# Kernel optimization log

Hardware: AMD Instinct MI355X
Metric: run time of the kernel (lower is better)

Reference implementation:

```python
import jax, jax.numpy as jnp
import numpy as np

NITER = 3

def fft2c(x):
    x = jnp.fft.ifftshift(x, axes=(-2, -1))
    x = jnp.fft.fft2(x, axes=(-2, -1), norm='ortho')
    return jnp.fft.fftshift(x, axes=(-2, -1))

def ifft2c(x):
    x = jnp.fft.ifftshift(x, axes=(-2, -1))
    x = jnp.fft.ifft2(x, axes=(-2, -1), norm='ortho')
    return jnp.fft.fftshift(x, axes=(-2, -1))

def conv3d(x, w):
    # x: [N, D, H, W, C]; w: [3,3,3,Cin,Cout]; 'same' padding, stride 1, no bias
    return jax.lax.conv_general_dilated(x, w, window_strides=(1, 1, 1), padding='SAME',
                                        dimension_numbers=('NDHWC', 'DHWIO', 'NDHWC'))

def setup_inputs():
    key = jax.random.key(0)
    ks = jax.random.split(key, 16)
    nb, nt, nx, ny = 1, 18, 160, 160
    s = 0.05  # weight scale to keep unrolled iterations numerically tame
    d_real = jax.random.normal(ks[0], (nb, nt, nx, ny), jnp.float32)
    d_imag = jax.random.normal(ks[1], (nb, nt, nx, ny), jnp.float32)
    mask = jax.random.randint(ks[2], (nt, nx, ny), 0, 2, jnp.int32)
    W1 = jax.random.normal(ks[3], (NITER, 3, 3, 3, 2, 16), jnp.float32) * s
    W2 = jax.random.normal(ks[4], (NITER, 3, 3, 3, 16, 16), jnp.float32) * s
    W3 = jax.random.normal(ks[5], (NITER, 3, 3, 3, 16, 16), jnp.float32) * s
    W4 = jax.random.normal(ks[6], (NITER, 3, 3, 3, 16, 16), jnp.float32) * s
    W5 = jax.random.normal(ks[7], (NITER, 3, 3, 3, 16, 16), jnp.float32) * s
    W6 = jax.random.normal(ks[8], (NITER, 3, 3, 3, 16, 2), jnp.float32) * s
    lam1 = jnp.full((NITER,), 0.1, jnp.float32)       # lambda_step init
    lam2 = jnp.full((NITER,), 0.1, jnp.float32)       # lambda_step_2 init
    soft_thr = jnp.full((NITER,), 0.1, jnp.float32)
    thres_coef = jnp.full((NITER,), -2.0, jnp.float32)
    eta = jnp.full((NITER,), 0.01, jnp.float32)
    return dict(d_real=d_real, d_imag=d_imag, mask=mask, W1=W1, W2=W2, W3=W3, W4=W4,
                W5=W5, W6=W6, lam1=lam1, lam2=lam2, soft_thr=soft_thr,
                thres_coef=thres_coef, eta=eta)

def _slr_net(d_real, d_imag, mask, W1, W2, W3, W4, W5, W6, lam1, lam2, soft_thr, thres_coef, eta):
    d = jax.lax.complex(d_real, d_imag)          # [nb,nt,nx,ny] complex64
    m = mask.astype(jnp.complex64)               # [nt,nx,ny], broadcasts over batch
    x_rec = ifft2c(d * m)                        # E^H d
    t = jnp.zeros_like(x_rec)
    beta = jnp.zeros_like(x_rec)
    X_SYM = []
    for i in range(NITER):
        lam = jnp.maximum(lam1[i], 0.0).astype(jnp.complex64)
        lam2c = jnp.maximum(lam2[i], 0.0).astype(jnp.complex64)
        # data-consistency gradient: E^H (E x - d)
        ATAX = ifft2c(m * (m * fft2c(x_rec) - d))
        r_n = x_rec - lam * ATAX + lam2c * (x_rec + beta - t)
        r = jnp.stack([r_n.real, r_n.imag], axis=-1)  # [nb,nt,nx,ny,2]
        x1 = jax.nn.relu(conv3d(r, W1[i]))
        x2 = jax.nn.relu(conv3d(x1, W2[i]))
        x3 = conv3d(x2, W3[i])
        x_soft = jnp.sign(x3) * jax.nn.relu(jnp.abs(x3) - soft_thr[i])
        x4 = jax.nn.relu(conv3d(x_soft, W4[i]))
        x5 = jax.nn.relu(conv3d(x4, W5[i]))
        x6 = conv3d(x5, W6[i])
        x_out = x6 + r
        xs = jax.nn.relu(conv3d(x3, W4[i]))
        xs = jax.nn.relu(conv3d(xs, W5[i]))
        xs = conv3d(xs, W6[i])
        x_sym = xs - r
        x_rec = jax.lax.complex(x_out[..., 0], x_out[..., 1])
        # low-rank step: batched thin SVD with learned singular-value thresholding
        nb_, nt_, nx_, ny_ = x_rec.shape
        M = x_rec.reshape(nb_, nt_, nx_ * ny_)
        U, S, Vh = jnp.linalg.svd(M, full_matrices=False)   # U:[b,nt,nt] S:[b,nt] Vh:[b,nt,nx*ny]
        thres = jax.nn.sigmoid(thres_coef[i]) * S[:, :1]
        S = jax.nn.relu(S - thres)
        t = (U * S[:, None, :].astype(U.dtype)) @ Vh
        t = t.reshape(nb_, nt_, nx_, ny_)
        beta = beta + jnp.maximum(eta[i], 0.0).astype(jnp.complex64) * (x_rec - t)
        X_SYM.append(x_sym)
    return x_rec, jnp.stack(X_SYM)

def reference(d_real, d_imag, mask, W1, W2, W3, W4, W5, W6, lam1, lam2, soft_thr, thres_coef, eta):
    return _slr_net(d_real, d_imag, mask, W1, W2, W3, W4, W5, W6, lam1, lam2, soft_thr, thres_coef, eta)
```

## Files before the change

kernel.cpp:

```cpp
#include <hip/hip_runtime.h>
#include <hip/hip_fp16.h>

#define NT 18
#define NX 160
#define NY 160
#define NPIX (NX*NY)
#define NVOX (NT*NPIX)

typedef _Float16 __attribute__((ext_vector_type(2))) half2t;
typedef _Float16 __attribute__((ext_vector_type(8))) half8t;
typedef float    __attribute__((ext_vector_type(4))) f32x4;
typedef unsigned int u32;
typedef __attribute__((address_space(1))) const u32 gu32;
typedef __attribute__((address_space(3))) u32 lu32;

__global__ void probe_kernel(float* __restrict__ out, int n, float val) {
  int i = blockIdx.x * 256 + threadIdx.x;
  if (i < n) out[i] = val;
}

__global__ void make_g_kernel(float2* __restrict__ G) {
  int idx = blockIdx.x * 256 + threadIdx.x;
  if (idx >= NPIX) return;
  int r = idx / NY, c = idx - (idx / NY) * NY;
  int rs = (r + 80) % 160;
  int cs = (c + 80) % 160;
  int prod = (rs * cs) % 160;
  double ang = -2.0 * 3.14159265358979323846 * (double)prod / 160.0;
  double sc = 0.07905694150420949;
  G[idx] = make_float2((float)(cos(ang) * sc), (float)(sin(ang) * sc));
}

__global__ void zero_kernel(float* __restrict__ p, int n) {
  int i = blockIdx.x * 256 + threadIdx.x;
  if (i < n) p[i] = 0.f;
}

template <int MASKD>
__global__ void fft_pass_last4(const float2* __restrict__ in, float2* __restrict__ out,
                               const float2* __restrict__ G, int conjf,
                               const float* __restrict__ dr, const float* __restrict__ di,
                               const int* __restrict__ maskp) {
  __shared__ float2 rows[4][NY];
  int r0 = blockIdx.x * 4;
  int v = threadIdx.x;
#pragma unroll
  for (int r = 0; r < 4; ++r) {
    size_t idx = (size_t)(r0 + r) * NY + v;
    if (MASKD) {
      float m = (float)maskp[idx];
      rows[r][v] = make_float2(m * dr[idx], m * di[idx]);
    } else {
      rows[r][v] = in[idx];
    }
  }
  __syncthreads();
  float sgn = conjf ? -1.f : 1.f;
  float ar[4] = {0.f, 0.f, 0.f, 0.f}, ai[4] = {0.f, 0.f, 0.f, 0.f};
  for (int k = 0; k < NY; ++k) {
    float2 g = G[k * NY + v];
    float gi = sgn * g.y;
#pragma unroll
    for (int r = 0; r < 4; ++r) {
      float2 a = rows[r][k];
      ar[r] += a.x * g.x - a.y * gi;
      ai[r] += a.x * gi + a.y * g.x;
    }
  }
#pragma unroll
  for (int r = 0; r < 4; ++r)
    out[(size_t)(r0 + r) * NY + v] = make_float2(ar[r], ai[r]);
}

template <int EPI>
__global__ void fft_pass_mid4(const float2* __restrict__ in, void* __restrict__ outv,
                              const float2* __restrict__ G, int conjf,
                              const float* __restrict__ dr, const float* __restrict__ di,
                              const int* __restrict__ maskp,
                              const float2* __restrict__ xrec2, const float2* __restrict__ beta2,
                              const float2* __restrict__ tbuf2,
                              const float* __restrict__ l1p, const float* __restrict__ l2p) {
  __shared__ float2 grow[4][NX];
  int b = (int)blockIdx.x;
  int sb = (b & 7) * 90 + (b >> 3);
  int t = sb / 40;
  int u0 = (sb - t * 40) * 4;
  int v = threadIdx.x;
#pragma unroll
  for (int r = 0; r < 4; ++r) grow[r][v] = G[(u0 + r) * NX + v];
  __syncthreads();
  float sgn = conjf ? -1.f : 1.f;
  float ar[4] = {0.f, 0.f, 0.f, 0.f}, ai[4] = {0.f, 0.f, 0.f, 0.f};
  const float2* base = in + (size_t)t * NPIX;
  for (int j = 0; j < NX; ++j) {
    float2 a = base[j * NY + v];
#pragma unroll
    for (int r = 0; r < 4; ++r) {
      float2 g = grow[r][j];
      float gi = sgn * g.y;
      ar[r] += a.x * g.x - a.y * gi;
      ai[r] += a.x * gi + a.y * g.x;
    }
  }
  float l1 = 0.f, l2 = 0.f;
  if (EPI == 2) { l1 = fmaxf(l1p[0], 0.f); l2 = fmaxf(l2p[0], 0.f); }
#pragma unroll
  for (int r = 0; r < 4; ++r) {
    size_t idx = (size_t)t * NPIX + (size_t)(u0 + r) * NY + v;
    if (EPI == 0) {
      ((float2*)outv)[idx] = make_float2(ar[r], ai[r]);
    } else if (EPI == 1) {
      float m = (float)maskp[idx];
      ((float2*)outv)[idx] = make_float2(m * (m * ar[r] - dr[idx]),
                                         m * (m * ai[r] - di[idx]));
    } else {
      float2 x = xrec2[idx], bb = beta2[idx], tt = tbuf2[idx];
      ((float*)outv)[2 * idx]     = (1.f + l2) * x.x - l1 * ar[r] + l2 * (bb.x - tt.x);
      ((float*)outv)[2 * idx + 1] = (1.f + l2) * x.y - l1 * ai[r] + l2 * (bb.y - tt.y);
    }
  }
}

template <int MODE>
__device__ void eigen_part(const float2* __restrict__ Ain, float* __restrict__ scr,
                           const float* __restrict__ tcp, float2* __restrict__ Wout) {
  __shared__ float Ar[NT][NT], Ai_[NT][NT], Vr[NT][NT], Vi_[NT][NT];
  __shared__ float cS[9], sS[9], erS[9], eiS[9];
  __shared__ int pS[9], qS[9];
  __shared__ float ratio[NT];
  int tid = threadIdx.x;
  for (int idx = tid; idx < NT * NT; idx += 256) {
    int i = idx / NT, j = idx - (idx / NT) * NT;
    if (MODE == 1) {
      float2 a = Ain[idx];
      Ar[i][j] = a.x;
      Ai_[i][j] = (i == j) ? 0.f : a.y;
      Vr[i][j] = (i == j) ? 1.f : 0.f;
      Vi_[i][j] = 0.f;
    } else {
      Ar[i][j] = scr[idx];
      Ai_[i][j] = scr[324 + idx];
      Vr[i][j] = scr[648 + idx];
      Vi_[i][j] = scr[972 + idx];
    }
  }
  __syncthreads();
  for (int sweep = 0; sweep < 2; ++sweep) {
    for (int r = 0; r < NT - 1; ++r) {
      if (tid < 9) {
        int k = tid;
        int a = (r + k) % (NT - 1);
        int b = (k == 0) ? (NT - 1) : (r - k + (NT - 1)) % (NT - 1);
        int p = min(a, b), q = max(a, b);
        pS[k] = p; qS[k] = q;
        float apr = Ar[p][q], api = Ai_[p][q];
        float r2 = apr * apr + api * api;
        float c = 1.f, s = 0.f, er = 1.f, ei = 0.f;
        if (r2 > 1e-28f) {
          float rr = sqrtf(r2);
          float inv_r = 1.f / rr;
          er = apr * inv_r; ei = api * inv_r;
          float th = (Ar[q][q] - Ar[p][p]) * 0.5f * inv_r;
          float tt = (th >= 0.f ? 1.f : -1.f) / (fabsf(th) + sqrtf(th * th + 1.f));
          c = 1.f / sqrtf(tt * tt + 1.f);
          s = tt * c;
        }
        cS[k] = c; sS[k] = s; erS[k] = er; eiS[k] = ei;
      }
      __syncthreads();
      if (tid < 9 * NT) {
        int idx = tid;
        int k = idx / 9, j = idx - (idx / 9) * 9;
        int p = pS[j], q = qS[j];
        float c = cS[j], s = sS[j], er = erS[j], ei = eiS[j];
        float apr = Ar[k][p], api = Ai_[k][p];
        float aqr = Ar[k][q], aqi = Ai_[k][q];
        float eqr = er * aqr + ei * aqi;
        float eqi = er * aqi - ei * aqr;
        Ar[k][p] = c * apr - s * eqr;  Ai_[k][p] = c * api - s * eqi;
        Ar[k][q] = s * apr + c * eqr;  Ai_[k][q] = s * api + c * eqi;
        float vpr = Vr[k][p], vpi = Vi_[k][p];
        float vqr = Vr[k][q], vqi = Vi_[k][q];
        float evr = er * vqr + ei * vqi;
        float evi = er * vqi - ei * vqr;
        Vr[k][p] = c * vpr - s * evr;  Vi_[k][p] = c * vpi - s * evi;
        Vr[k][q] = s * vpr + c * evr;  Vi_[k][q] = s * vpi + c * evi;
      }
      __syncthreads();
      if (tid < 9 * NT) {
        int idx = tid;
        int k = idx / 9, j = idx - (idx / 9) * 9;
        int p = pS[j], q = qS[j];
        float c = cS[j], s = sS[j], er = erS[j], ei = eiS[j];
        float bpr = Ar[p][k], bpi = Ai_[p][k];
        float bqr = Ar[q][k], bqi = Ai_[q][k];
        float ebr = er * bqr - ei * bqi;
        float ebi = er * bqi + ei * bqr;
        Ar[p][k] = c * bpr - s * ebr;  Ai_[p][k] = c * bpi - s * ebi;
        Ar[q][k] = s * bpr + c * ebr;  Ai_[q][k] = s * bpi + c * ebi;
      }
      __syncthreads();
    }
  }
  if (MODE == 3) {
    if (tid == 0) {
      float smax = 0.f;
      for (int k = 0; k < NT; ++k) {
        float sv = sqrtf(fmaxf(Ar[k][k], 0.f));
        ratio[k] = sv;
        smax = fmaxf(smax, sv);
      }
      float sig = 1.f / (1.f + expf(-tcp[0]));
      float thres = sig * smax;
      for (int k = 0; k < NT; ++k) {
        float sv = ratio[k];
        ratio[k] = (sv > thres) ? (sv - thres) / sv : 0.f;
      }
    }
    __syncthreads();
    for (int idx = tid; idx < NT * NT; idx += 256) {
      int i = idx / NT, j = idx - (idx / NT) * NT;
      float wr = 0.f, wi = 0.f;
      for (int k = 0; k < NT; ++k) {
        float rk = ratio[k];
        wr += rk * (Vr[i][k] * Vr[j][k] + Vi_[i][k] * Vi_[j][k]);
        wi += rk * (Vi_[i][k] * Vr[j][k] - Vr[i][k] * Vi_[j][k]);
      }
      Wout[idx] = make_float2(wr, wi);
    }
  } else {
    for (int idx = tid; idx < NT * NT; idx += 256) {
      int i = idx / NT, j = idx - (idx / NT) * NT;
      scr[idx]       = Ar[i][j];
      scr[324 + idx] = Ai_[i][j];
      scr[648 + idx] = Vr[i][j];
      scr[972 + idx] = Vi_[i][j];
    }
  }
}

template <int COUT, bool RELU, int OUTMODE, bool SOFT, int EIG>
__global__ void __launch_bounds__(256)
conv3d_mfma_kernel(const __half* __restrict__ in_, const float* __restrict__ wts,
                   void* __restrict__ out_, const float* __restrict__ res, float resSign,
                   const float* __restrict__ thrp,
                   const float2* __restrict__ eigA, float* __restrict__ eigScr,
                   const float* __restrict__ tcp, float2* __restrict__ eigW,
                   float* __restrict__ outReal) {
  if constexpr (EIG > 0) {
    if (blockIdx.x == 0) { eigen_part<EIG>(eigA, eigScr, tcp, eigW); return; }
  }
  __shared__ alignas(16) __half lds[12 * 2592];
  const int tid = threadIdx.x;
  const int bid0 = (EIG > 0) ? ((int)blockIdx.x - 1) : (int)blockIdx.x;
  const int bid = (bid0 & 7) * 180 + (bid0 >> 3);
  const int z  = bid / 80;
  const int y0 = (bid - z * 80) * 2;

  const int lane = tid & 63;
  const int wv = tid >> 6;
  const int n = lane & 15;
  const int g = lane >> 4;
  const int sel = g >> 1;
  const int ci = (g & 1) * 8;

  half8t bw[14];
#pragma unroll
  for (int c = 0; c < 14; ++c) {
#pragma unroll
    for (int j = 0; j < 8; ++j) {
      int kg = c * 32 + g * 8 + j;
      float w = (kg < 432 && n < COUT) ? wts[kg * COUT + n] : 0.f;
      bw[c][j] = (_Float16)w;
    }
  }

  if constexpr (!SOFT) {
    half8t zero8 = {0, 0, 0, 0, 0, 0, 0, 0};
    if (tid < 48) {
      int row = tid >> 2, which = tid & 3;
      int off = (which < 2) ? which : (320 + which);
      *reinterpret_cast<half8t*>(&lds[(row * 324 + off) * 8]) = zero8;
    }
#pragma unroll 1
    for (int row = 0; row < 12; ++row) {
      int zz = z - 1 + (row >> 2);
      int yy = y0 - 1 + (row & 3);
      if ((unsigned)zz >= (unsigned)NT || (unsigned)yy >= (unsigned)NX) {
        for (int i = tid; i < 324; i += 256)
          *reinterpret_cast<half8t*>(&lds[(row * 324 + i) * 8]) = zero8;
      }
    }
    const int wb = tid & ~63;
#pragma unroll 1
    for (int base = 0; base < 3888; base += 256) {
      int i = base + tid;
      if (i < 3888) {
        int row = i / 324;
        int off = i - row * 324;
        int zz = z - 1 + (row >> 2);
        int yy = y0 - 1 + (row & 3);
        bool valid = (off >= 2) && (off < 322) &&
                     ((unsigned)zz < (unsigned)NT) && ((unsigned)yy < (unsigned)NX);
        if (valid) {
          const __half* src = in_ + (size_t)((zz * NX + yy) * NY) * 16 + (size_t)(off - 2) * 8;
          __builtin_amdgcn_global_load_lds(
              (gu32*)(const void*)src,
              (lu32*)(void*)&lds[(size_t)(base + wb) * 8],
              16, 0, 0);
        }
      }
    }
  } else {
    float thr = thrp[0];
    for (int i = tid; i < 3888; i += 256) {
      int row = i / 324;
      int off = i - row * 324;
      int zz = z - 1 + (row >> 2);
      int yy = y0 - 1 + (row & 3);
      half8t v = {0, 0, 0, 0, 0, 0, 0, 0};
      if (off >= 2 && off < 322 && (unsigned)zz < (unsigned)NT && (unsigned)yy < (unsigned)NX) {
        int xx = (off - 2) >> 1;
        int cih = (off - 2) & 1;
        v = *reinterpret_cast<const half8t*>(
              in_ + ((size_t)((zz * NX + yy) * NY + xx)) * 16 + cih * 8);
#pragma unroll
        for (int e = 0; e < 8; ++e) {
          float f = (float)v[e];
          v[e] = (_Float16)copysignf(fmaxf(fabsf(f) - thr, 0.f), f);
        }
      }
      *reinterpret_cast<half8t*>(&lds[row * 2592 + off * 8]) = v;
    }
  }
  __syncthreads();

#pragma unroll 1
  for (int t = 0; t < 5; ++t) {
    int tl = wv * 5 + t;
    int yloc = (tl >= 10) ? 1 : 0;
    int x0 = (tl - yloc * 10) * 16;

    f32x4 acc = {0.f, 0.f, 0.f, 0.f};
#pragma unroll
    for (int c = 0; c < 14; ++c) {
      const int t0 = 2 * c, t1 = 2 * c + 1;
      const int dz0 = t0 / 9, dy0 = (t0 / 3) % 3, dx0 = t0 % 3;
      const int dz1 = t1 / 9, dy1 = (t1 / 3) % 3, dx1 = t1 % 3;
      half8t a = {0, 0, 0, 0, 0, 0, 0, 0};
      if (c < 13 || !sel) {
        int dz = sel ? dz1 : dz0;
        int dy = sel ? dy1 : dy0;
        int dx = sel ? dx1 : dx0;
        int rowi = dz * 4 + yloc + dy;
        int aoff = rowi * 2592 + (x0 + n + dx) * 16 + ci;
        a = *reinterpret_cast<const half8t*>(&lds[aoff]);
      }
      acc = __builtin_amdgcn_mfma_f32_16x16x32_f16(a, bw[c], acc, 0, 0, 0);
    }

    size_t vb = ((size_t)(z * NX) + (y0 + yloc)) * NY + x0;
    if (n < COUT) {
#pragma unroll
      for (int r = 0; r < 4; ++r) {
        float v = acc[r];
        size_t oidx = (vb + g * 4 + r) * COUT + n;
        if (res) v += resSign * res[oidx];
        if (RELU) v = fmaxf(v, 0.f);
        if (OUTMODE == 1) ((__half*)out_)[oidx] = __float2half(v);
        else {
          ((float*)out_)[oidx] = v;
          if (COUT == 2 && outReal && n == 0) outReal[vb + g * 4 + r] = v;
        }
      }
    }
  }
}

template <bool RELU>
__global__ void __launch_bounds__(256)
conv3d_mfma2in_kernel(const float* __restrict__ in_, const float* __restrict__ wts,
                      __half* __restrict__ out_) {
  __shared__ alignas(8) __half lds2[12 * 324];
  const int tid = threadIdx.x;
  const int bid0 = (int)blockIdx.x;
  const int bid = (bid0 & 7) * 180 + (bid0 >> 3);
  const int z  = bid / 80;
  const int y0 = (bid - z * 80) * 2;
  const int lane = tid & 63;
  const int wv = tid >> 6;
  const int n = lane & 15;
  const int g = lane >> 4;

  half8t bw[2];
#pragma unroll
  for (int c = 0; c < 2; ++c) {
#pragma unroll
    for (int j = 0; j < 8; ++j) {
      int k = c * 32 + g * 8 + j;
      float w = (k < 54) ? wts[k * 16 + n] : 0.f;
      bw[c][j] = (_Float16)w;
    }
  }

  for (int i = tid; i < 12 * 162; i += 256) {
    int row = i / 162;
    int vox = i - row * 162;
    int zz = z - 1 + (row >> 2);
    int yy = y0 - 1 + (row & 3);
    int xx = vox - 1;
    half2t v2 = {(_Float16)0.f, (_Float16)0.f};
    if ((unsigned)zz < (unsigned)NT && (unsigned)yy < (unsigned)NX && (unsigned)xx < (unsigned)NY) {
      float2 f = reinterpret_cast<const float2*>(in_)[(size_t)(zz * NX + yy) * NY + xx];
      v2[0] = (_Float16)f.x;
      v2[1] = (_Float16)f.y;
    }
    *reinterpret_cast<half2t*>(&lds2[i * 2]) = v2;
  }
  __syncthreads();

#pragma unroll 1
  for (int t = 0; t < 5; ++t) {
    int tl = wv * 5 + t;
    int yloc = (tl >= 10) ? 1 : 0;
    int x0 = (tl - yloc * 10) * 16;
    f32x4 acc = {0.f, 0.f, 0.f, 0.f};
#pragma unroll
    for (int c = 0; c < 2; ++c) {
      half8t a = {0, 0, 0, 0, 0, 0, 0, 0};
#pragma unroll
      for (int u = 0; u < 4; ++u) {
        int tap = c * 16 + g * 4 + u;
        if (tap < 27) {
          int dz = tap / 9, dy = (tap / 3) % 3, dx = tap % 3;
          int rowi = dz * 4 + yloc + dy;
          half2t p = *reinterpret_cast<const half2t*>(&lds2[rowi * 324 + (x0 + n + dx) * 2]);
          a[2 * u] = p[0];
          a[2 * u + 1] = p[1];
        }
      }
      acc = __builtin_amdgcn_mfma_f32_16x16x32_f16(a, bw[c], acc, 0, 0, 0);
    }
    size_t vb = ((size_t)(z * NX) + (y0 + yloc)) * NY + x0;
#pragma unroll
    for (int r = 0; r < 4; ++r) {
      float v = acc[r];
      if (RELU) v = fmaxf(v, 0.f);
      out_[(vb + g * 4 + r) * 16 + n] = __float2half(v);
    }
  }
}

__global__ void gram_kernel(const float2* __restrict__ M, float2* __restrict__ A) {
  int b = blockIdx.x;
  int i = 0;
  while (b >= NT - i) { b -= NT - i; ++i; }
  int j = i + b;
  int tid = threadIdx.x;
  float sr = 0.f, si = 0.f;
  for (int p = tid; p < NPIX; p += 256) {
    float2 a = M[(size_t)i * NPIX + p];
    float2 c = M[(size_t)j * NPIX + p];
    sr += a.x * c.x + a.y * c.y;
    si += a.y * c.x - a.x * c.y;
  }
  __shared__ float rs[256], is_[256];
  rs[tid] = sr; is_[tid] = si;
  __syncthreads();
  for (int s = 128; s > 0; s >>= 1) {
    if (tid < s) { rs[tid] += rs[tid + s]; is_[tid] += is_[tid + s]; }
    __syncthreads();
  }
  if (tid == 0) {
    A[i * NT + j] = make_float2(rs[0], is_[0]);
    if (i != j) A[j * NT + i] = make_float2(rs[0], -is_[0]);
  }
}

__global__ void svd_apply_kernel(const float2* __restrict__ M, const float2* __restrict__ Wm,
                                 float2* __restrict__ t, float2* __restrict__ beta,
                                 const float* __restrict__ etap) {
  __shared__ float2 W[NT * NT];
  int tid = threadIdx.x;
  for (int i = tid; i < NT * NT; i += 256) W[i] = Wm[i];
  __syncthreads();
  int p = blockIdx.x * 256 + tid;
  float eta = fmaxf(etap[0], 0.f);
  float2 m[NT];
#pragma unroll
  for (int j = 0; j < NT; ++j) m[j] = M[(size_t)j * NPIX + p];
#pragma unroll
  for (int i = 0; i < NT; ++i) {
    float tr = 0.f, ti = 0.f;
#pragma unroll
    for (int j = 0; j < NT; ++j) {
      float2 w = W[i * NT + j];
      tr += w.x * m[j].x - w.y * m[j].y;
      ti += w.x * m[j].y + w.y * m[j].x;
    }
    t[(size_t)i * NPIX + p] = make_float2(tr, ti);
    float2 b = beta[(size_t)i * NPIX + p];
    b.x += eta * (m[i].x - tr);
    b.y += eta * (m[i].y - ti);
    beta[(size_t)i * NPIX + p] = b;
  }
}

extern "C" void kernel_launch(void* const* d_in, const int* in_sizes, int n_in,
                              void* d_out, int out_size, void* d_ws, size_t ws_size,
                              hipStream_t stream) {
  const float* d_real    = (const float*)d_in[0];
  const float* d_imag    = (const float*)d_in[1];
  const int*   mask      = (const int*)d_in[2];
  const float* W1        = (const float*)d_in[3];
  const float* W2        = (const float*)d_in[4];
  const float* W3        = (const float*)d_in[5];
  const float* W4        = (const float*)d_in[6];
  const float* W5        = (const float*)d_in[7];
  const float* W6        = (const float*)d_in[8];
  const float* lam1      = (const float*)d_in[9];
  const float* lam2      = (const float*)d_in[10];
  const float* soft_thr  = (const float*)d_in[11];
  const float* thres_c   = (const float*)d_in[12];
  const float* eta       = (const float*)d_in[13];
  float* out = (float*)d_out;
  (void)in_sizes; (void)n_in;

  const size_t NEEDED = 59400000ull;
  if (ws_size < NEEDED) {
    probe_kernel<<<(out_size + 255) / 256, 256, 0, stream>>>(out, out_size,
                                                             (float)(ws_size >> 20));
    return;
  }

  char* wp_ = (char*)d_ws;
  auto alloc = [&](size_t bytes) {
    char* r = wp_;
    wp_ += (bytes + 255) & ~(size_t)255;
    return r;
  };
  float2* G      = (float2*)alloc((size_t)NPIX * sizeof(float2));
  float2* xrec   = (float2*)alloc((size_t)NVOX * sizeof(float2));
  float2* tbuf   = (float2*)alloc((size_t)NVOX * sizeof(float2));
  float2* beta   = (float2*)alloc((size_t)NVOX * sizeof(float2));
  float*  Rf     = (float*)alloc((size_t)NVOX * 2 * sizeof(float));
  __half* Af     = (__half*)alloc((size_t)NVOX * 16 * sizeof(__half));
  __half* Bf     = (__half*)alloc((size_t)NVOX * 16 * sizeof(__half));
  __half* Cf     = (__half*)alloc((size_t)NVOX * 16 * sizeof(__half));
  float2* Agram  = (float2*)alloc((size_t)NT * NT * sizeof(float2));
  float2* Wmat   = (float2*)alloc((size_t)NT * NT * sizeof(float2));
  float*  EigScr = (float*)alloc(1296 * sizeof(float));
  float2* T1 = (float2*)Af;
  float2* T2 = (float2*)Bf;

  make_g_kernel<<<100, 256, 0, stream>>>(G);
  zero_kernel<<<7200, 256, 0, stream>>>((float*)tbuf, 4 * NVOX);

  fft_pass_last4<1><<<720, 160, 0, stream>>>(nullptr, T2, G, 1, d_real, d_imag, mask);
  fft_pass_mid4<0><<<720, 160, 0, stream>>>(T2, xrec, G, 1, nullptr, nullptr, nullptr,
                                            nullptr, nullptr, nullptr, nullptr, nullptr);

  for (int i = 0; i < 3; ++i) {
    fft_pass_last4<0><<<720, 160, 0, stream>>>(xrec, T1, G, 0, nullptr, nullptr, nullptr);
    fft_pass_mid4<1><<<720, 160, 0, stream>>>(T1, T2, G, 0, d_real, d_imag, mask,
                                              nullptr, nullptr, nullptr, nullptr, nullptr);
    fft_pass_last4<0><<<720, 160, 0, stream>>>(T2, T1, G, 1, nullptr, nullptr, nullptr);
    fft_pass_mid4<2><<<720, 160, 0, stream>>>(T1, Rf, G, 1, nullptr, nullptr, nullptr,
                                              xrec, beta, tbuf, lam1 + i, lam2 + i);
    conv3d_mfma2in_kernel<true><<<1440, 256, 0, stream>>>(Rf, W1 + (size_t)i * 864, Af);
    conv3d_mfma_kernel<16, true, 1, false, 0><<<1440, 256, 0, stream>>>(
        Af, W2 + (size_t)i * 6912, Bf, nullptr, 0.f, nullptr,
        nullptr, nullptr, nullptr, nullptr, nullptr);
    conv3d_mfma_kernel<16, false, 1, false, 0><<<1440, 256, 0, stream>>>(
        Bf, W3 + (size_t)i * 6912, Cf, nullptr, 0.f, nullptr,
        nullptr, nullptr, nullptr, nullptr, nullptr);
    conv3d_mfma_kernel<16, true, 1, true, 0><<<1440, 256, 0, stream>>>(
        Cf, W4 + (size_t)i * 6912, Bf, nullptr, 0.f, soft_thr + i,
        nullptr, nullptr, nullptr, nullptr, nullptr);
    conv3d_mfma_kernel<16, true, 1, false, 0><<<1440, 256, 0, stream>>>(
        Bf, W5 + (size_t)i * 6912, Af, nullptr, 0.f, nullptr,
        nullptr, nullptr, nullptr, nullptr, nullptr);

    if (i < 2) {
      conv3d_mfma_kernel<2, false, 0, false, 0><<<1440, 256, 0, stream>>>(
          Af, W6 + (size_t)i * 864, (float*)xrec, Rf, 1.f, nullptr,
          nullptr, nullptr, nullptr, nullptr, nullptr);
      gram_kernel<<<171, 256, 0, stream>>>((const float2*)xrec, Agram);
      conv3d_mfma_kernel<16, true, 1, false, 1><<<1441, 256, 0, stream>>>(
          Cf, W4 + (size_t)i * 6912, Bf, nullptr, 0.f, nullptr,
          Agram, EigScr, thres_c + i, Wmat, nullptr);
      conv3d_mfma_kernel<16, true, 1, false, 2><<<1441, 256, 0, stream>>>(
          Bf, W5 + (size_t)i * 6912, Af, nullptr, 0.f, nullptr,
          Agram, EigScr, thres_c + i, Wmat, nullptr);
      conv3d_mfma_kernel<2, false, 0, false, 3><<<1441, 256, 0, stream>>>(
          Af, W6 + (size_t)i * 864, out + 460800 + (size_t)921600 * i, Rf, -1.f, nullptr,
          Agram, EigScr, thres_c + i, Wmat, nullptr);
      svd_apply_kernel<<<100, 256, 0, stream>>>((const float2*)xrec, Wmat, tbuf, beta, eta + i);
    } else {
      conv3d_mfma_kernel<2, false, 0, false, 0><<<1440, 256, 0, stream>>>(
          Af, W6 + (size_t)i * 864, (float*)xrec, Rf, 1.f, nullptr,
          nullptr, nullptr, nullptr, nullptr, out);
      conv3d_mfma_kernel<16, true, 1, false, 0><<<1440, 256, 0, stream>>>(
          Cf, W4 + (size_t)i * 6912, Bf, nullptr, 0.f, nullptr,
          nullptr, nullptr, nullptr, nullptr, nullptr);
      conv3d_mfma_kernel<16, true, 1, false, 0><<<1440, 256, 0, stream>>>(
          Bf, W5 + (size_t)i * 6912, Af, nullptr, 0.f, nullptr,
          nullptr, nullptr, nullptr, nullptr, nullptr);
      conv3d_mfma_kernel<2, false, 0, false, 0><<<1440, 256, 0, stream>>>(
          Af, W6 + (size_t)i * 864, out + 460800 + (size_t)921600 * i, Rf, -1.f, nullptr,
          nullptr, nullptr, nullptr, nullptr, nullptr);
    }
  }
}
```

Baseline: 1.383 ms.

## Retile conv3d blocks to 4 rows by 80 columns to cut halo loads

Each conv block previously covered two full 160-wide output rows and staged a 3x4-row halo in LDS. It now covers four output rows by half a row width (80 columns), with each wave owning one row, so it stages a 3x6-row, 82-column halo. That drops the y-halo overhead from 2x to 1.5x per output row at the cost of a small x-halo, which lowers global and LDS traffic per output. LDS use per block shrinks slightly and the block count stays the same.

```diff
diff --git a/kernel.cpp b/kernel.cpp
--- a/kernel.cpp
+++ b/kernel.cpp
@@ -239,6 +239,10 @@
   }
 }
 
+#define ROWCH 164
+#define NROWS 18
+#define NCHUNK (NROWS*ROWCH)
+
 template <int COUT, bool RELU, int OUTMODE, bool SOFT, int EIG>
 __global__ void __launch_bounds__(256)
 conv3d_mfma_kernel(const __half* __restrict__ in_, const float* __restrict__ wts,
@@ -250,12 +254,14 @@
   if constexpr (EIG > 0) {
     if (blockIdx.x == 0) { eigen_part<EIG>(eigA, eigScr, tcp, eigW); return; }
   }
-  __shared__ alignas(16) __half lds[12 * 2592];
+  __shared__ alignas(16) __half lds[NCHUNK * 8];
   const int tid = threadIdx.x;
   const int bid0 = (EIG > 0) ? ((int)blockIdx.x - 1) : (int)blockIdx.x;
   const int bid = (bid0 & 7) * 180 + (bid0 >> 3);
-  const int z  = bid / 80;
-  const int y0 = (bid - z * 80) * 2;
+  const int z   = bid / 80;
+  const int rem = bid - z * 80;
+  const int y0  = (rem >> 1) * 4;
+  const int xbase = (rem & 1) * 80;
 
   const int lane = tid & 63;
   const int wv = tid >> 6;
@@ -277,33 +283,34 @@
 
   if constexpr (!SOFT) {
     half8t zero8 = {0, 0, 0, 0, 0, 0, 0, 0};
-    if (tid < 48) {
-      int row = tid >> 2, which = tid & 3;
-      int off = (which < 2) ? which : (320 + which);
-      *reinterpret_cast<half8t*>(&lds[(row * 324 + off) * 8]) = zero8;
+    if (tid < 2 * NROWS) {
+      int row = tid >> 1, which = tid & 1;
+      int off = (xbase == 0) ? which : (162 + which);
+      *reinterpret_cast<half8t*>(&lds[(row * ROWCH + off) * 8]) = zero8;
     }
 #pragma unroll 1
-    for (int row = 0; row < 12; ++row) {
-      int zz = z - 1 + (row >> 2);
-      int yy = y0 - 1 + (row & 3);
+    for (int row = 0; row < NROWS; ++row) {
+      int zz = z - 1 + row / 6;
+      int yy = y0 - 1 + row % 6;
       if ((unsigned)zz >= (unsigned)NT || (unsigned)yy >= (unsigned)NX) {
-        for (int i = tid; i < 324; i += 256)
-          *reinterpret_cast<half8t*>(&lds[(row * 324 + i) * 8]) = zero8;
+        for (int i = tid; i < ROWCH; i += 256)
+          *reinterpret_cast<half8t*>(&lds[(row * ROWCH + i) * 8]) = zero8;
       }
     }
     const int wb = tid & ~63;
 #pragma unroll 1
-    for (int base = 0; base < 3888; base += 256) {
+    for (int base = 0; base < NCHUNK; base += 256) {
       int i = base + tid;
-      if (i < 3888) {
-        int row = i / 324;
-        int off = i - row * 324;
-        int zz = z - 1 + (row >> 2);
-        int yy = y0 - 1 + (row & 3);
-        bool valid = (off >= 2) && (off < 322) &&
-                     ((unsigned)zz < (unsigned)NT) && ((unsigned)yy < (unsigned)NX);
+      if (i < NCHUNK) {
+        int row = i / ROWCH;
+        int off = i - row * ROWCH;
+        int zz = z - 1 + row / 6;
+        int yy = y0 - 1 + row % 6;
+        int x = xbase - 1 + (off >> 1);
+        bool valid = ((unsigned)zz < (unsigned)NT) && ((unsigned)yy < (unsigned)NX) &&
+                     ((unsigned)x < (unsigned)NY);
         if (valid) {
-          const __half* src = in_ + (size_t)((zz * NX + yy) * NY) * 16 + (size_t)(off - 2) * 8;
+          const __half* src = in_ + ((size_t)((zz * NX + yy) * NY + x)) * 16 + (off & 1) * 8;
           __builtin_amdgcn_global_load_lds(
               (gu32*)(const void*)src,
               (lu32*)(void*)&lds[(size_t)(base + wb) * 8],
@@ -313,33 +320,32 @@
     }
   } else {
     float thr = thrp[0];
-    for (int i = tid; i < 3888; i += 256) {
-      int row = i / 324;
-      int off = i - row * 324;
-      int zz = z - 1 + (row >> 2);
-      int yy = y0 - 1 + (row & 3);
+    for (int i = tid; i < NCHUNK; i += 256) {
+      int row = i / ROWCH;
+      int off = i - row * ROWCH;
+      int zz = z - 1 + row / 6;
+      int yy = y0 - 1 + row % 6;
+      int x = xbase - 1 + (off >> 1);
       half8t v = {0, 0, 0, 0, 0, 0, 0, 0};
-      if (off >= 2 && off < 322 && (unsigned)zz < (unsigned)NT && (unsigned)yy < (unsigned)NX) {
-        int xx = (off - 2) >> 1;
-        int cih = (off - 2) & 1;
+      if ((unsigned)zz < (unsigned)NT && (unsigned)yy < (unsigned)NX &&
+          (unsigned)x < (unsigned)NY) {
         v = *reinterpret_cast<const half8t*>(
-              in_ + ((size_t)((zz * NX + yy) * NY + xx)) * 16 + cih * 8);
+              in_ + ((size_t)((zz * NX + yy) * NY + x)) * 16 + (off & 1) * 8);
 #pragma unroll
         for (int e = 0; e < 8; ++e) {
           float f = (float)v[e];
           v[e] = (_Float16)copysignf(fmaxf(fabsf(f) - thr, 0.f), f);
         }
       }
-      *reinterpret_cast<half8t*>(&lds[row * 2592 + off * 8]) = v;
+      *reinterpret_cast<half8t*>(&lds[(size_t)i * 8]) = v;
     }
   }
   __syncthreads();
 
+  const int yloc = wv;
 #pragma unroll 1
   for (int t = 0; t < 5; ++t) {
-    int tl = wv * 5 + t;
-    int yloc = (tl >= 10) ? 1 : 0;
-    int x0 = (tl - yloc * 10) * 16;
+    int xloc = t * 16;
 
     f32x4 acc = {0.f, 0.f, 0.f, 0.f};
 #pragma unroll
@@ -352,14 +358,15 @@
         int dz = sel ? dz1 : dz0;
         int dy = sel ? dy1 : dy0;
         int dx = sel ? dx1 : dx0;
-        int rowi = dz * 4 + yloc + dy;
-        int aoff = rowi * 2592 + (x0 + n + dx) * 16 + ci;
+        int rowi = dz * 6 + yloc + dy;
+        int slot = xloc + n + dx;
+        int aoff = rowi * (ROWCH * 8) + slot * 16 + ci;
         a = *reinterpret_cast<const half8t*>(&lds[aoff]);
       }
       acc = __builtin_amdgcn_mfma_f32_16x16x32_f16(a, bw[c], acc, 0, 0, 0);
     }
 
-    size_t vb = ((size_t)(z * NX) + (y0 + yloc)) * NY + x0;
+    size_t vb = ((size_t)(z * NX) + (y0 + yloc)) * NY + xbase + xloc;
     if (n < COUT) {
 #pragma unroll
       for (int r = 0; r < 4; ++r) {
```

Result: faster. 1.219 ms (-11.9%).
